# Kernel tuning notes

Measured on AMD Instinct MI355X. Metric: run time of the kernel, lower is better.

The kernel has to match this reference:

```python
import jax, jax.numpy as jnp
import numpy as np

EPS = 1e-5

def _conv1d(x, w, b):
    # x: [B, T, Cin]; w: [Cout, Cin, K] (torch layout); padding=1, stride=1
    y = jax.lax.conv_general_dilated(
        x, jnp.transpose(w, (2, 1, 0)), window_strides=(1,), padding=[(1, 1)],
        dimension_numbers=('NWC', 'WIO', 'NWC'))
    return y + b

def _layernorm(x, g, b):
    mu = jnp.mean(x, axis=-1, keepdims=True)
    var = jnp.mean(jnp.square(x - mu), axis=-1, keepdims=True)
    return (x - mu) * jax.lax.rsqrt(var + EPS) * g + b

def _predictor(x, conv1_w, conv1_b, ln1_g, ln1_b, conv2_w, conv2_b, ln2_g, ln2_b, lin_w, lin_b):
    h = _layernorm(jax.nn.relu(_conv1d(x, conv1_w, conv1_b)), ln1_g, ln1_b)
    h = _layernorm(jax.nn.relu(_conv1d(h, conv2_w, conv2_b)), ln2_g, ln2_b)
    # linear to 1 channel, relu, squeeze -> [B, T]
    return jax.nn.relu(jnp.einsum('btf,f->bt', h, lin_w[:, 0]) + lin_b[0])

def _length_regulate(x, durations, mel_max_length):
    # Equivalent to the one-hot alignment matmul: output frame p of batch b
    # copies token k where cumsum(dur)[k-1] <= p < cumsum(dur)[k]; zeros beyond total.
    B, T, D = x.shape
    cum = jnp.cumsum(durations, axis=-1)                       # [B, T]
    frames = jnp.arange(mel_max_length, dtype=cum.dtype)       # [M]
    idx = jax.vmap(lambda c: jnp.searchsorted(c, frames, side='right'))(cum)  # [B, M]
    idx = jnp.clip(idx, 0, T - 1)
    out = jnp.take_along_axis(x, idx[..., None], axis=1)       # [B, M, D]
    mask = (frames[None, :] < cum[:, -1:])                     # [B, M]
    return out * mask[..., None].astype(x.dtype)

def setup_inputs() -> dict:
    key = jax.random.key(0)
    ks = jax.random.split(key, 8)
    B, T, D, F = 32, 512, 256, 256
    M = 3584  # mel_max_length >= max possible sum of durations (7 * 512)
    x = jax.random.normal(ks[0], (B, T, D), dtype=jnp.float32)
    target = jax.random.randint(ks[1], (B, T), 0, 8, dtype=jnp.int32)
    s = 0.02
    return {
        'x': x,
        'conv1_w': jax.random.normal(ks[2], (F, D, 3), jnp.float32) * s,
        'conv1_b': jnp.zeros((F,), jnp.float32),
        'ln1_g': jnp.ones((F,), jnp.float32),
        'ln1_b': jnp.zeros((F,), jnp.float32),
        'conv2_w': jax.random.normal(ks[3], (F, F, 3), jnp.float32) * s,
        'conv2_b': jnp.zeros((F,), jnp.float32),
        'ln2_g': jnp.ones((F,), jnp.float32),
        'ln2_b': jnp.zeros((F,), jnp.float32),
        'lin_w': jax.random.normal(ks[4], (F, 1), jnp.float32) * s,
        'lin_b': jnp.zeros((1,), jnp.float32),
        'target': target,
        'mel_max_length': M,
    }

def reference(x, conv1_w, conv1_b, ln1_g, ln1_b, conv2_w, conv2_b, ln2_g, ln2_b, lin_w, lin_b, target, mel_max_length):
    dur_pred = _predictor(x, conv1_w, conv1_b, ln1_g, ln1_b, conv2_w, conv2_b, ln2_g, ln2_b, lin_w, lin_b)
    output = _length_regulate(x, target, mel_max_length)
    return output, dur_pred
```

## Files before the change

kernel.cpp:

```cpp
#include <hip/hip_runtime.h>
#include <hip/hip_bf16.h>

typedef float f32x4 __attribute__((ext_vector_type(4)));
typedef __bf16 bf16x8 __attribute__((ext_vector_type(8)));

static __device__ __forceinline__ unsigned short f2bf(float f) {
    unsigned int u = __float_as_uint(f);
    unsigned int r = (u + 0x7fffu + ((u >> 16) & 1u)) >> 16;
    return (unsigned short)r;
}

static __device__ __forceinline__ void gll16(const void* g, void* l) {
    __builtin_amdgcn_global_load_lds(
        (const __attribute__((address_space(1))) unsigned int*)g,
        (__attribute__((address_space(3))) unsigned int*)l, 16, 0, 0);
}

__global__ __launch_bounds__(512) void prep(
    const float* __restrict__ w1, const float* __restrict__ w2,
    unsigned short* __restrict__ w1p, unsigned short* __restrict__ w2p,
    const int* __restrict__ tgt, short* __restrict__ idxT, int M)
{
    int blk = blockIdx.x;
    if (blk < 256) {
        int gi = blk * 512 + threadIdx.x;
        const float* w = (gi < 65536) ? w1 : w2;
        unsigned short* wp = (gi < 65536) ? w1p : w2p;
        int p = gi & 65535;
        int n = p >> 8, cin = p & 255;
        const float* src = w + (size_t)p * 3;
        float a[3] = {src[0], src[1], src[2]};
        int nb = n >> 4, nl = n & 15;
        int e = cin & 7, lhi = (cin >> 3) & 3, chi = cin >> 5;
        int base = nb * 512 + (lhi * 16 + nl) * 8 + e;
        #pragma unroll
        for (int kk = 0; kk < 3; ++kk)
            wp[(kk * 8 + chi) * 8192 + base] = f2bf(a[kk]);
    } else {
        __shared__ int s[512];
        int b = blk - 256, tid = threadIdx.x;
        int d = tgt[b * 512 + tid];
        s[tid] = d;
        __syncthreads();
        for (int off = 1; off < 512; off <<= 1) {
            int v = (tid >= off) ? s[tid - off] : 0;
            __syncthreads();
            s[tid] += v;
            __syncthreads();
        }
        int myend = s[tid];
        int mystart = myend - d;
        short* row = idxT + (size_t)b * M;
        for (int p = mystart; p < myend; ++p) row[p] = (short)tid;
        __syncthreads();
        int total = s[511];
        for (int p = total + tid; p < M; p += 512) row[p] = (short)-1;
    }
}

static __device__ __forceinline__ void gather_part(
    int gblk, int jpb, int base, const float* __restrict__ x,
    const short* __restrict__ idxT, float* __restrict__ out, int M,
    int wv, int lane)
{
    int b = gblk / jpb;
    int r0 = (gblk - b * jpb) * 32 + base;
    const short* row = idxT + (size_t)b * M;
    int id[4];
    #pragma unroll
    for (int i = 0; i < 4; ++i) id[i] = row[r0 + i * 8 + wv];
    #pragma unroll
    for (int i = 0; i < 4; ++i) {
        int m = r0 + i * 8 + wv;
        float4 v = make_float4(0.f, 0.f, 0.f, 0.f);
        if (id[i] >= 0)
            v = *reinterpret_cast<const float4*>(x + ((size_t)(b * 512 + id[i])) * 256 + lane * 4);
        *reinterpret_cast<float4*>(out + ((size_t)b * M + m) * 256 + lane * 4) = v;
    }
}

__global__ __launch_bounds__(512, 4) void conv1_hetero(
    const float* __restrict__ x, const unsigned short* __restrict__ Wp,
    const float* __restrict__ bias, const float* __restrict__ g,
    const float* __restrict__ be, unsigned short* __restrict__ h1b,
    const short* __restrict__ idxT, float* __restrict__ out, int M)
{
    __shared__ __align__(16) unsigned short As[66 * 256];
    __shared__ __align__(16) unsigned short Bsm[2][8192];
    __shared__ float lnS[4][64], lnQ[4][64];

    const int tid = threadIdx.x;
    const int lane = tid & 63;
    const int wv = tid >> 6;

    if (blockIdx.x >= 256) {
        gather_part(blockIdx.x - 256, 68, 0, x, idxT, out, M, wv, lane);
        return;
    }

    const int wmi = wv >> 2, wni = wv & 3;
    const int grp = lane >> 4, lr = lane & 15;
    const int b = blockIdx.x >> 3;
    const int t_base = (blockIdx.x & 7) * 64;

    #pragma unroll
    for (int i = 0; i < 9; ++i) {
        int cc = i * 512 + tid;
        if (cc < 66 * 64) {
            int row = cc >> 6, q = cc & 63;
            int tt = t_base - 1 + row;
            ushort4 o = make_ushort4(0, 0, 0, 0);
            if ((unsigned)tt < 512u) {
                float4 v = *reinterpret_cast<const float4*>(x + ((size_t)(b * 512 + tt)) * 256 + q * 4);
                o.x = f2bf(v.x); o.y = f2bf(v.y); o.z = f2bf(v.z); o.w = f2bf(v.w);
            }
            *reinterpret_cast<ushort4*>(&As[row * 256 + ((q * 4) ^ ((row & 7) << 3))]) = o;
        }
    }

    const char* wpB = (const char*)Wp;
    char* bs0 = (char*)&Bsm[0][0];
    #define STAGE_B(kt, buf) do {                                              \
        const char* _s = wpB + (kt) * 16384 + wv * 2048 + lane * 16;           \
        char* _d = bs0 + (buf) * 16384 + wv * 2048;                            \
        gll16(_s, _d); gll16(_s + 1024, _d + 1024);                            \
    } while (0)

    STAGE_B(0, 0);
    __syncthreads();

    f32x4 acc[2][4] = {};
    int cur = 0;
    for (int kt = 0; kt < 24; ++kt) {
        if (kt < 23) STAGE_B(kt + 1, cur ^ 1);
        const int kk = kt >> 3, cin0 = (kt & 7) * 32;
        bf16x8 af[2], bfr[4];
        #pragma unroll
        for (int mi = 0; mi < 2; ++mi) {
            int tr = wmi * 32 + mi * 16 + lr + kk;
            af[mi] = *reinterpret_cast<const bf16x8*>(&As[tr * 256 + ((cin0 + grp * 8) ^ ((tr & 7) << 3))]);
        }
        #pragma unroll
        for (int ni = 0; ni < 4; ++ni)
            bfr[ni] = *reinterpret_cast<const bf16x8*>(&Bsm[cur][(wni * 4 + ni) * 512 + lane * 8]);
        __builtin_amdgcn_s_setprio(1);
        #pragma unroll
        for (int mi = 0; mi < 2; ++mi)
            #pragma unroll
            for (int ni = 0; ni < 4; ++ni)
                acc[mi][ni] = __builtin_amdgcn_mfma_f32_16x16x32_bf16(af[mi], bfr[ni], acc[mi][ni], 0, 0, 0);
        __builtin_amdgcn_s_setprio(0);
        __syncthreads();
        cur ^= 1;
    }

    float bcol[4], gcol[4], becol[4];
    #pragma unroll
    for (int ni = 0; ni < 4; ++ni) {
        int col = wni * 64 + ni * 16 + lr;
        bcol[ni] = bias[col]; gcol[ni] = g[col]; becol[ni] = be[col];
    }
    #pragma unroll
    for (int mi = 0; mi < 2; ++mi)
        #pragma unroll
        for (int ni = 0; ni < 4; ++ni)
            #pragma unroll
            for (int r = 0; r < 4; ++r)
                acc[mi][ni][r] = fmaxf(acc[mi][ni][r] + bcol[ni], 0.f);

    #pragma unroll
    for (int mi = 0; mi < 2; ++mi)
        #pragma unroll
        for (int r = 0; r < 4; ++r) {
            float s = acc[mi][0][r] + acc[mi][1][r] + acc[mi][2][r] + acc[mi][3][r];
            float q = acc[mi][0][r] * acc[mi][0][r] + acc[mi][1][r] * acc[mi][1][r]
                    + acc[mi][2][r] * acc[mi][2][r] + acc[mi][3][r] * acc[mi][3][r];
            #pragma unroll
            for (int off = 1; off < 16; off <<= 1) {
                s += __shfl_xor(s, off);
                q += __shfl_xor(q, off);
            }
            if (lr == 0) {
                int R = wmi * 32 + mi * 16 + grp * 4 + r;
                lnS[wni][R] = s; lnQ[wni][R] = q;
            }
        }
    __syncthreads();

    unsigned short* Hs = &Bsm[0][0];
    #pragma unroll
    for (int mi = 0; mi < 2; ++mi)
        #pragma unroll
        for (int r = 0; r < 4; ++r) {
            int R = wmi * 32 + mi * 16 + grp * 4 + r;
            float mu = (lnS[0][R] + lnS[1][R] + lnS[2][R] + lnS[3][R]) * (1.f / 256.f);
            float var = (lnQ[0][R] + lnQ[1][R] + lnQ[2][R] + lnQ[3][R]) * (1.f / 256.f) - mu * mu;
            float rs = rsqrtf(var + 1e-5f);
            #pragma unroll
            for (int ni = 0; ni < 4; ++ni) {
                int col = wni * 64 + ni * 16 + lr;
                float h = (acc[mi][ni][r] - mu) * rs * gcol[ni] + becol[ni];
                Hs[R * 256 + (col ^ ((R & 7) << 3))] = f2bf(h);
            }
        }
    __syncthreads();
    #pragma unroll
    for (int i = 0; i < 4; ++i) {
        int c = i * 512 + tid;
        int row = c >> 5, seg = c & 31;
        uint4 v = *reinterpret_cast<const uint4*>(&Hs[row * 256 + seg * 8]);
        *reinterpret_cast<uint4*>(h1b + ((size_t)(b * 512 + t_base + row)) * 256 + seg * 8) = v;
    }
    #undef STAGE_B
}

__global__ __launch_bounds__(512, 4) void conv2_hetero(
    const unsigned short* __restrict__ h1b, const unsigned short* __restrict__ Wp,
    const float* __restrict__ bias, const float* __restrict__ g,
    const float* __restrict__ be, const float* __restrict__ lw,
    const float* __restrict__ lb, float* __restrict__ dur,
    const short* __restrict__ idxT, const float* __restrict__ x,
    float* __restrict__ out, int M)
{
    __shared__ __align__(16) unsigned short As[66 * 256];
    __shared__ __align__(16) unsigned short Bsm[2][8192];
    __shared__ float lnS[4][64], lnQ[4][64], lnD[4][64];

    const int tid = threadIdx.x;
    const int lane = tid & 63;
    const int wv = tid >> 6;

    if (blockIdx.x >= 256) {
        gather_part(blockIdx.x - 256, 44, 2176, x, idxT, out, M, wv, lane);
        return;
    }

    const int wmi = wv >> 2, wni = wv & 3;
    const int grp = lane >> 4, lr = lane & 15;
    const int b = blockIdx.x >> 3;
    const int t_base = (blockIdx.x & 7) * 64;

    {
        const char* src = (const char*)h1b + ((size_t)(b * 512 + t_base)) * 512 + wv * 4096 + lane * 16;
        char* dst = (char*)&As[256] + wv * 4096;
        #pragma unroll
        for (int i = 0; i < 4; ++i) gll16(src + i * 1024, dst + i * 1024);
    }
    if (tid < 32) {
        int tt = t_base - 1;
        uint4 v = make_uint4(0u, 0u, 0u, 0u);
        if (tt >= 0)
            v = *reinterpret_cast<const uint4*>((const char*)h1b + ((size_t)(b * 512 + tt)) * 512 + tid * 16);
        *reinterpret_cast<uint4*>((char*)As + tid * 16) = v;
    } else if (tid < 64) {
        int t2 = tid - 32, tt = t_base + 64;
        uint4 v = make_uint4(0u, 0u, 0u, 0u);
        if (tt < 512)
            v = *reinterpret_cast<const uint4*>((const char*)h1b + ((size_t)(b * 512 + tt)) * 512 + t2 * 16);
        *reinterpret_cast<uint4*>((char*)&As[65 * 256] + t2 * 16) = v;
    }

    const char* wpB = (const char*)Wp;
    char* bs0 = (char*)&Bsm[0][0];
    #define STAGE_B(kt, buf) do {                                              \
        const char* _s = wpB + (kt) * 16384 + wv * 2048 + lane * 16;           \
        char* _d = bs0 + (buf) * 16384 + wv * 2048;                            \
        gll16(_s, _d); gll16(_s + 1024, _d + 1024);                            \
    } while (0)

    STAGE_B(0, 0);
    __syncthreads();

    f32x4 acc[2][4] = {};
    int cur = 0;
    for (int kt = 0; kt < 24; ++kt) {
        if (kt < 23) STAGE_B(kt + 1, cur ^ 1);
        const int kk = kt >> 3, cin0 = (kt & 7) * 32;
        bf16x8 af[2], bfr[4];
        #pragma unroll
        for (int mi = 0; mi < 2; ++mi) {
            int tr = wmi * 32 + mi * 16 + lr + kk;
            af[mi] = *reinterpret_cast<const bf16x8*>(&As[tr * 256 + ((cin0 + grp * 8) ^ (((tr + 7) & 7) << 3))]);
        }
        #pragma unroll
        for (int ni = 0; ni < 4; ++ni)
            bfr[ni] = *reinterpret_cast<const bf16x8*>(&Bsm[cur][(wni * 4 + ni) * 512 + lane * 8]);
        __builtin_amdgcn_s_setprio(1);
        #pragma unroll
        for (int mi = 0; mi < 2; ++mi)
            #pragma unroll
            for (int ni = 0; ni < 4; ++ni)
                acc[mi][ni] = __builtin_amdgcn_mfma_f32_16x16x32_bf16(af[mi], bfr[ni], acc[mi][ni], 0, 0, 0);
        __builtin_amdgcn_s_setprio(0);
        __syncthreads();
        cur ^= 1;
    }

    float bcol[4], gcol[4], becol[4], wcol[4];
    #pragma unroll
    for (int ni = 0; ni < 4; ++ni) {
        int col = wni * 64 + ni * 16 + lr;
        bcol[ni] = bias[col]; gcol[ni] = g[col]; becol[ni] = be[col]; wcol[ni] = lw[col];
    }
    #pragma unroll
    for (int mi = 0; mi < 2; ++mi)
        #pragma unroll
        for (int ni = 0; ni < 4; ++ni)
            #pragma unroll
            for (int r = 0; r < 4; ++r)
                acc[mi][ni][r] = fmaxf(acc[mi][ni][r] + bcol[ni], 0.f);

    #pragma unroll
    for (int mi = 0; mi < 2; ++mi)
        #pragma unroll
        for (int r = 0; r < 4; ++r) {
            float s = acc[mi][0][r] + acc[mi][1][r] + acc[mi][2][r] + acc[mi][3][r];
            float q = acc[mi][0][r] * acc[mi][0][r] + acc[mi][1][r] * acc[mi][1][r]
                    + acc[mi][2][r] * acc[mi][2][r] + acc[mi][3][r] * acc[mi][3][r];
            #pragma unroll
            for (int off = 1; off < 16; off <<= 1) {
                s += __shfl_xor(s, off);
                q += __shfl_xor(q, off);
            }
            if (lr == 0) {
                int R = wmi * 32 + mi * 16 + grp * 4 + r;
                lnS[wni][R] = s; lnQ[wni][R] = q;
            }
        }
    __syncthreads();
    #pragma unroll
    for (int mi = 0; mi < 2; ++mi)
        #pragma unroll
        for (int r = 0; r < 4; ++r) {
            int R = wmi * 32 + mi * 16 + grp * 4 + r;
            float mu = (lnS[0][R] + lnS[1][R] + lnS[2][R] + lnS[3][R]) * (1.f / 256.f);
            float var = (lnQ[0][R] + lnQ[1][R] + lnQ[2][R] + lnQ[3][R]) * (1.f / 256.f) - mu * mu;
            float rs = rsqrtf(var + 1e-5f);
            float d = ((acc[mi][0][r] - mu) * rs * gcol[0] + becol[0]) * wcol[0]
                    + ((acc[mi][1][r] - mu) * rs * gcol[1] + becol[1]) * wcol[1]
                    + ((acc[mi][2][r] - mu) * rs * gcol[2] + becol[2]) * wcol[2]
                    + ((acc[mi][3][r] - mu) * rs * gcol[3] + becol[3]) * wcol[3];
            #pragma unroll
            for (int off = 1; off < 16; off <<= 1) d += __shfl_xor(d, off);
            if (lr == 0) lnD[wni][R] = d;
        }
    __syncthreads();
    if (tid < 64) {
        float dd = lnD[0][tid] + lnD[1][tid] + lnD[2][tid] + lnD[3][tid] + lb[0];
        dur[(size_t)b * 512 + t_base + tid] = fmaxf(dd, 0.f);
    }
    #undef STAGE_B
}

extern "C" void kernel_launch(void* const* d_in, const int* in_sizes, int n_in,
                              void* d_out, int out_size, void* d_ws, size_t ws_size,
                              hipStream_t stream) {
    const float* x   = (const float*)d_in[0];
    const float* w1  = (const float*)d_in[1];
    const float* b1  = (const float*)d_in[2];
    const float* g1  = (const float*)d_in[3];
    const float* be1 = (const float*)d_in[4];
    const float* w2  = (const float*)d_in[5];
    const float* b2  = (const float*)d_in[6];
    const float* g2  = (const float*)d_in[7];
    const float* be2 = (const float*)d_in[8];
    const float* lw  = (const float*)d_in[9];
    const float* lb  = (const float*)d_in[10];
    const int* tgt   = (const int*)d_in[11];
    float* out = (float*)d_out;

    const int B = 32, T = 512, C = 256;
    const int rows = B * T;
    const int M = (out_size - rows) / (B * C);

    char* ws = (char*)d_ws;
    unsigned short* w1p = (unsigned short*)(ws);
    unsigned short* w2p = (unsigned short*)(ws + 393216);
    unsigned short* h1b = (unsigned short*)(ws + 786432);
    short* idxT         = (short*)(ws + 9175040);

    prep<<<288, 512, 0, stream>>>(w1, w2, w1p, w2p, tgt, idxT, M);
    conv1_hetero<<<2432, 512, 0, stream>>>(x, w1p, b1, g1, be1, h1b, idxT, out, M);
    conv2_hetero<<<1664, 512, 0, stream>>>(h1b, w2p, b2, g2, be2, lw, lb,
                                           out + (size_t)B * M * C, idxT, x, out, M);
}
```

Measured before the change: 57.97 us.

## Split conv A-tile staging into two channel halves to halve LDS footprint

Both conv kernels now stage the activation tile in two 128-channel halves instead of loading all 256 channels at once. This halves the As shared buffer so LDS use per block drops, which may let more blocks or gather work fit per CU. The K loop is reordered so each half runs 12 steps over the matching weight tiles. The cost is an extra tile reload, an extra barrier, and a pipeline restart between halves.

```diff
diff --git a/kernel.cpp b/kernel.cpp
--- a/kernel.cpp
+++ b/kernel.cpp
@@ -85,7 +85,7 @@
     const float* __restrict__ be, unsigned short* __restrict__ h1b,
     const short* __restrict__ idxT, float* __restrict__ out, int M)
 {
-    __shared__ __align__(16) unsigned short As[66 * 256];
+    __shared__ __align__(16) unsigned short As[66 * 128];
     __shared__ __align__(16) unsigned short Bsm[2][8192];
     __shared__ float lnS[4][64], lnQ[4][64];
 
@@ -103,55 +103,62 @@
     const int b = blockIdx.x >> 3;
     const int t_base = (blockIdx.x & 7) * 64;
 
-    #pragma unroll
-    for (int i = 0; i < 9; ++i) {
-        int cc = i * 512 + tid;
-        if (cc < 66 * 64) {
-            int row = cc >> 6, q = cc & 63;
-            int tt = t_base - 1 + row;
-            ushort4 o = make_ushort4(0, 0, 0, 0);
-            if ((unsigned)tt < 512u) {
-                float4 v = *reinterpret_cast<const float4*>(x + ((size_t)(b * 512 + tt)) * 256 + q * 4);
-                o.x = f2bf(v.x); o.y = f2bf(v.y); o.z = f2bf(v.z); o.w = f2bf(v.w);
-            }
-            *reinterpret_cast<ushort4*>(&As[row * 256 + ((q * 4) ^ ((row & 7) << 3))]) = o;
-        }
-    }
-
     const char* wpB = (const char*)Wp;
     char* bs0 = (char*)&Bsm[0][0];
-    #define STAGE_B(kt, buf) do {                                              \
-        const char* _s = wpB + (kt) * 16384 + wv * 2048 + lane * 16;           \
+    #define STAGE_B(ktg, buf) do {                                             \
+        const char* _s = wpB + (ktg) * 16384 + wv * 2048 + lane * 16;          \
         char* _d = bs0 + (buf) * 16384 + wv * 2048;                            \
         gll16(_s, _d); gll16(_s + 1024, _d + 1024);                            \
     } while (0)
 
-    STAGE_B(0, 0);
-    __syncthreads();
-
     f32x4 acc[2][4] = {};
     int cur = 0;
-    for (int kt = 0; kt < 24; ++kt) {
-        if (kt < 23) STAGE_B(kt + 1, cur ^ 1);
-        const int kk = kt >> 3, cin0 = (kt & 7) * 32;
-        bf16x8 af[2], bfr[4];
-        #pragma unroll
-        for (int mi = 0; mi < 2; ++mi) {
-            int tr = wmi * 32 + mi * 16 + lr + kk;
-            af[mi] = *reinterpret_cast<const bf16x8*>(&As[tr * 256 + ((cin0 + grp * 8) ^ ((tr & 7) << 3))]);
-        }
-        #pragma unroll
-        for (int ni = 0; ni < 4; ++ni)
-            bfr[ni] = *reinterpret_cast<const bf16x8*>(&Bsm[cur][(wni * 4 + ni) * 512 + lane * 8]);
-        __builtin_amdgcn_s_setprio(1);
-        #pragma unroll
-        for (int mi = 0; mi < 2; ++mi)
+
+    for (int h = 0; h < 2; ++h) {
+        #pragma unroll
+        for (int i = 0; i < 5; ++i) {
+            int cc = i * 512 + tid;
+            if (cc < 66 * 32) {
+                int row = cc >> 5, ql = cc & 31;
+                int tt = t_base - 1 + row;
+                ushort4 o = make_ushort4(0, 0, 0, 0);
+                if ((unsigned)tt < 512u) {
+                    float4 v = *reinterpret_cast<const float4*>(
+                        x + ((size_t)(b * 512 + tt)) * 256 + h * 128 + ql * 4);
+                    o.x = f2bf(v.x); o.y = f2bf(v.y); o.z = f2bf(v.z); o.w = f2bf(v.w);
+                }
+                *reinterpret_cast<ushort4*>(&As[row * 128 + ((ql * 4) ^ ((row & 7) << 3))]) = o;
+            }
+        }
+        STAGE_B(h * 4, cur);
+        __syncthreads();
+
+        for (int j = 0; j < 12; ++j) {
+            if (j < 11) {
+                int jn = j + 1;
+                STAGE_B((jn >> 2) * 8 + h * 4 + (jn & 3), cur ^ 1);
+            }
+            const int cbl = j & 3, kk = j >> 2;
+            bf16x8 af[2], bfr[4];
+            #pragma unroll
+            for (int mi = 0; mi < 2; ++mi) {
+                int tr = wmi * 32 + mi * 16 + lr + kk;
+                af[mi] = *reinterpret_cast<const bf16x8*>(
+                    &As[tr * 128 + ((cbl * 32 + grp * 8) ^ ((tr & 7) << 3))]);
+            }
             #pragma unroll
             for (int ni = 0; ni < 4; ++ni)
-                acc[mi][ni] = __builtin_amdgcn_mfma_f32_16x16x32_bf16(af[mi], bfr[ni], acc[mi][ni], 0, 0, 0);
-        __builtin_amdgcn_s_setprio(0);
-        __syncthreads();
-        cur ^= 1;
+                bfr[ni] = *reinterpret_cast<const bf16x8*>(&Bsm[cur][(wni * 4 + ni) * 512 + lane * 8]);
+            __builtin_amdgcn_s_setprio(1);
+            #pragma unroll
+            for (int mi = 0; mi < 2; ++mi)
+                #pragma unroll
+                for (int ni = 0; ni < 4; ++ni)
+                    acc[mi][ni] = __builtin_amdgcn_mfma_f32_16x16x32_bf16(af[mi], bfr[ni], acc[mi][ni], 0, 0, 0);
+            __builtin_amdgcn_s_setprio(0);
+            __syncthreads();
+            cur ^= 1;
+        }
     }
 
     float bcol[4], gcol[4], becol[4];
@@ -199,8 +206,8 @@
             #pragma unroll
             for (int ni = 0; ni < 4; ++ni) {
                 int col = wni * 64 + ni * 16 + lr;
-                float h = (acc[mi][ni][r] - mu) * rs * gcol[ni] + becol[ni];
-                Hs[R * 256 + (col ^ ((R & 7) << 3))] = f2bf(h);
+                float hv = (acc[mi][ni][r] - mu) * rs * gcol[ni] + becol[ni];
+                Hs[R * 256 + (col ^ ((R & 7) << 3))] = f2bf(hv);
             }
         }
     __syncthreads();
@@ -222,7 +229,7 @@
     const short* __restrict__ idxT, const float* __restrict__ x,
     float* __restrict__ out, int M)
 {
-    __shared__ __align__(16) unsigned short As[66 * 256];
+    __shared__ __align__(16) unsigned short As[66 * 128];
     __shared__ __align__(16) unsigned short Bsm[2][8192];
     __shared__ float lnS[4][64], lnQ[4][64], lnD[4][64];
 
@@ -240,60 +247,69 @@
     const int b = blockIdx.x >> 3;
     const int t_base = (blockIdx.x & 7) * 64;
 
-    {
-        const char* src = (const char*)h1b + ((size_t)(b * 512 + t_base)) * 512 + wv * 4096 + lane * 16;
-        char* dst = (char*)&As[256] + wv * 4096;
-        #pragma unroll
-        for (int i = 0; i < 4; ++i) gll16(src + i * 1024, dst + i * 1024);
-    }
-    if (tid < 32) {
-        int tt = t_base - 1;
-        uint4 v = make_uint4(0u, 0u, 0u, 0u);
-        if (tt >= 0)
-            v = *reinterpret_cast<const uint4*>((const char*)h1b + ((size_t)(b * 512 + tt)) * 512 + tid * 16);
-        *reinterpret_cast<uint4*>((char*)As + tid * 16) = v;
-    } else if (tid < 64) {
-        int t2 = tid - 32, tt = t_base + 64;
-        uint4 v = make_uint4(0u, 0u, 0u, 0u);
-        if (tt < 512)
-            v = *reinterpret_cast<const uint4*>((const char*)h1b + ((size_t)(b * 512 + tt)) * 512 + t2 * 16);
-        *reinterpret_cast<uint4*>((char*)&As[65 * 256] + t2 * 16) = v;
-    }
-
     const char* wpB = (const char*)Wp;
+    const char* h1B = (const char*)h1b;
     char* bs0 = (char*)&Bsm[0][0];
-    #define STAGE_B(kt, buf) do {                                              \
-        const char* _s = wpB + (kt) * 16384 + wv * 2048 + lane * 16;           \
+    #define STAGE_B(ktg, buf) do {                                             \
+        const char* _s = wpB + (ktg) * 16384 + wv * 2048 + lane * 16;          \
         char* _d = bs0 + (buf) * 16384 + wv * 2048;                            \
         gll16(_s, _d); gll16(_s + 1024, _d + 1024);                            \
     } while (0)
 
-    STAGE_B(0, 0);
-    __syncthreads();
-
     f32x4 acc[2][4] = {};
     int cur = 0;
-    for (int kt = 0; kt < 24; ++kt) {
-        if (kt < 23) STAGE_B(kt + 1, cur ^ 1);
-        const int kk = kt >> 3, cin0 = (kt & 7) * 32;
-        bf16x8 af[2], bfr[4];
-        #pragma unroll
-        for (int mi = 0; mi < 2; ++mi) {
-            int tr = wmi * 32 + mi * 16 + lr + kk;
-            af[mi] = *reinterpret_cast<const bf16x8*>(&As[tr * 256 + ((cin0 + grp * 8) ^ (((tr + 7) & 7) << 3))]);
-        }
-        #pragma unroll
-        for (int ni = 0; ni < 4; ++ni)
-            bfr[ni] = *reinterpret_cast<const bf16x8*>(&Bsm[cur][(wni * 4 + ni) * 512 + lane * 8]);
-        __builtin_amdgcn_s_setprio(1);
-        #pragma unroll
-        for (int mi = 0; mi < 2; ++mi)
+
+    for (int h = 0; h < 2; ++h) {
+        #pragma unroll
+        for (int j2 = 0; j2 < 2; ++j2) {
+            int row0 = 1 + wv * 8 + j2 * 4;
+            const char* src = h1B
+                + ((size_t)(b * 512 + t_base + wv * 8 + j2 * 4 + (lane >> 4))) * 512
+                + h * 256 + (lane & 15) * 16;
+            gll16(src, (char*)As + row0 * 256);
+        }
+        if (tid < 16) {
+            int tt = t_base - 1;
+            uint4 v = make_uint4(0u, 0u, 0u, 0u);
+            if (tt >= 0)
+                v = *reinterpret_cast<const uint4*>(h1B + ((size_t)(b * 512 + tt)) * 512 + h * 256 + tid * 16);
+            *reinterpret_cast<uint4*>((char*)As + tid * 16) = v;
+        } else if (tid < 32) {
+            int t2 = tid - 16, tt = t_base + 64;
+            uint4 v = make_uint4(0u, 0u, 0u, 0u);
+            if (tt < 512)
+                v = *reinterpret_cast<const uint4*>(h1B + ((size_t)(b * 512 + tt)) * 512 + h * 256 + t2 * 16);
+            *reinterpret_cast<uint4*>((char*)As + 65 * 256 + t2 * 16) = v;
+        }
+        STAGE_B(h * 4, cur);
+        __syncthreads();
+
+        for (int j = 0; j < 12; ++j) {
+            if (j < 11) {
+                int jn = j + 1;
+                STAGE_B((jn >> 2) * 8 + h * 4 + (jn & 3), cur ^ 1);
+            }
+            const int cbl = j & 3, kk = j >> 2;
+            bf16x8 af[2], bfr[4];
+            #pragma unroll
+            for (int mi = 0; mi < 2; ++mi) {
+                int tr = wmi * 32 + mi * 16 + lr + kk;
+                af[mi] = *reinterpret_cast<const bf16x8*>(
+                    &As[tr * 128 + ((cbl * 32 + grp * 8) ^ (((tr + 7) & 7) << 3))]);
+            }
             #pragma unroll
             for (int ni = 0; ni < 4; ++ni)
-                acc[mi][ni] = __builtin_amdgcn_mfma_f32_16x16x32_bf16(af[mi], bfr[ni], acc[mi][ni], 0, 0, 0);
-        __builtin_amdgcn_s_setprio(0);
-        __syncthreads();
-        cur ^= 1;
+                bfr[ni] = *reinterpret_cast<const bf16x8*>(&Bsm[cur][(wni * 4 + ni) * 512 + lane * 8]);
+            __builtin_amdgcn_s_setprio(1);
+            #pragma unroll
+            for (int mi = 0; mi < 2; ++mi)
+                #pragma unroll
+                for (int ni = 0; ni < 4; ++ni)
+                    acc[mi][ni] = __builtin_amdgcn_mfma_f32_16x16x32_bf16(af[mi], bfr[ni], acc[mi][ni], 0, 0, 0);
+            __builtin_amdgcn_s_setprio(0);
+            __syncthreads();
+            cur ^= 1;
+        }
     }
 
     float bcol[4], gcol[4], becol[4], wcol[4];
```

Measured after the change: 57.87 us. Within noise of the previous version (-0.2%).

## Fuse both conv+layernorm stages into one kernel with halo recompute

Applied to the files above, without the earlier changes.

Merges the conv1 and conv2 kernels into a single kernel. Each block computes conv1 over 64 rows (62 outputs plus a halo on each side) and keeps the normalized intermediate in shared memory, so the bf16 h1 round-trip through global memory and one kernel launch go away. The conv1 input is staged in four 64-channel chunks to fit LDS, and the gather work is rebalanced into 64-row chunks appended after 288 compute blocks. The cost is about 3% extra conv1 compute for the halo rows and higher LDS use per block, which may reduce occupancy.

```diff
diff --git a/kernel.cpp b/kernel.cpp
--- a/kernel.cpp
+++ b/kernel.cpp
@@ -58,296 +58,253 @@
     }
 }
 
-static __device__ __forceinline__ void gather_part(
-    int gblk, int jpb, int base, const float* __restrict__ x,
-    const short* __restrict__ idxT, float* __restrict__ out, int M,
-    int wv, int lane)
+__global__ __launch_bounds__(512, 4) void fused(
+    const float* __restrict__ x,
+    const unsigned short* __restrict__ w1p, const float* __restrict__ b1,
+    const float* __restrict__ g1, const float* __restrict__ be1,
+    const unsigned short* __restrict__ w2p, const float* __restrict__ b2,
+    const float* __restrict__ g2, const float* __restrict__ be2,
+    const float* __restrict__ lw, const float* __restrict__ lb,
+    float* __restrict__ dur, const short* __restrict__ idxT,
+    float* __restrict__ out, int M)
 {
-    int b = gblk / jpb;
-    int r0 = (gblk - b * jpb) * 32 + base;
-    const short* row = idxT + (size_t)b * M;
-    int id[4];
-    #pragma unroll
-    for (int i = 0; i < 4; ++i) id[i] = row[r0 + i * 8 + wv];
-    #pragma unroll
-    for (int i = 0; i < 4; ++i) {
-        int m = r0 + i * 8 + wv;
-        float4 v = make_float4(0.f, 0.f, 0.f, 0.f);
-        if (id[i] >= 0)
-            v = *reinterpret_cast<const float4*>(x + ((size_t)(b * 512 + id[i])) * 256 + lane * 4);
-        *reinterpret_cast<float4*>(out + ((size_t)b * M + m) * 256 + lane * 4) = v;
-    }
-}
-
-__global__ __launch_bounds__(512, 4) void conv1_hetero(
-    const float* __restrict__ x, const unsigned short* __restrict__ Wp,
-    const float* __restrict__ bias, const float* __restrict__ g,
-    const float* __restrict__ be, unsigned short* __restrict__ h1b,
-    const short* __restrict__ idxT, float* __restrict__ out, int M)
-{
-    __shared__ __align__(16) unsigned short As[66 * 256];
+    __shared__ __align__(16) unsigned short H[64 * 256];
+    __shared__ __align__(16) unsigned short As[66 * 64];
     __shared__ __align__(16) unsigned short Bsm[2][8192];
-    __shared__ float lnS[4][64], lnQ[4][64];
+    __shared__ float lnS[4][64], lnQ[4][64], lnD[4][64];
 
     const int tid = threadIdx.x;
     const int lane = tid & 63;
     const int wv = tid >> 6;
 
-    if (blockIdx.x >= 256) {
-        gather_part(blockIdx.x - 256, 68, 0, x, idxT, out, M, wv, lane);
+    if (blockIdx.x >= 288) {
+        int gid = blockIdx.x - 288;
+        int b = gid / 56;
+        int r0 = (gid - b * 56) * 64;
+        const short* row = idxT + (size_t)b * M;
+        int id[8];
+        #pragma unroll
+        for (int i = 0; i < 8; ++i) id[i] = row[r0 + i * 8 + wv];
+        #pragma unroll
+        for (int i = 0; i < 8; ++i) {
+            int m = r0 + i * 8 + wv;
+            float4 v = make_float4(0.f, 0.f, 0.f, 0.f);
+            if (id[i] >= 0)
+                v = *reinterpret_cast<const float4*>(x + ((size_t)(b * 512 + id[i])) * 256 + lane * 4);
+            *reinterpret_cast<float4*>(out + ((size_t)b * M + m) * 256 + lane * 4) = v;
+        }
         return;
     }
 
     const int wmi = wv >> 2, wni = wv & 3;
     const int grp = lane >> 4, lr = lane & 15;
-    const int b = blockIdx.x >> 3;
-    const int t_base = (blockIdx.x & 7) * 64;
-
-    #pragma unroll
-    for (int i = 0; i < 9; ++i) {
-        int cc = i * 512 + tid;
-        if (cc < 66 * 64) {
-            int row = cc >> 6, q = cc & 63;
-            int tt = t_base - 1 + row;
-            ushort4 o = make_ushort4(0, 0, 0, 0);
-            if ((unsigned)tt < 512u) {
-                float4 v = *reinterpret_cast<const float4*>(x + ((size_t)(b * 512 + tt)) * 256 + q * 4);
-                o.x = f2bf(v.x); o.y = f2bf(v.y); o.z = f2bf(v.z); o.w = f2bf(v.w);
-            }
-            *reinterpret_cast<ushort4*>(&As[row * 256 + ((q * 4) ^ ((row & 7) << 3))]) = o;
-        }
-    }
-
-    const char* wpB = (const char*)Wp;
+    const int b = blockIdx.x / 9;
+    const int t0 = (blockIdx.x - b * 9) * 62;
+
     char* bs0 = (char*)&Bsm[0][0];
-    #define STAGE_B(kt, buf) do {                                              \
-        const char* _s = wpB + (kt) * 16384 + wv * 2048 + lane * 16;           \
+    #define STAGE_B(basep, ktg, buf) do {                                      \
+        const char* _s = (const char*)(basep) + (ktg) * 16384 + wv * 2048 + lane * 16; \
         char* _d = bs0 + (buf) * 16384 + wv * 2048;                            \
         gll16(_s, _d); gll16(_s + 1024, _d + 1024);                            \
     } while (0)
 
-    STAGE_B(0, 0);
-    __syncthreads();
-
     f32x4 acc[2][4] = {};
     int cur = 0;
-    for (int kt = 0; kt < 24; ++kt) {
-        if (kt < 23) STAGE_B(kt + 1, cur ^ 1);
-        const int kk = kt >> 3, cin0 = (kt & 7) * 32;
-        bf16x8 af[2], bfr[4];
-        #pragma unroll
-        for (int mi = 0; mi < 2; ++mi) {
-            int tr = wmi * 32 + mi * 16 + lr + kk;
-            af[mi] = *reinterpret_cast<const bf16x8*>(&As[tr * 256 + ((cin0 + grp * 8) ^ ((tr & 7) << 3))]);
-        }
-        #pragma unroll
-        for (int ni = 0; ni < 4; ++ni)
-            bfr[ni] = *reinterpret_cast<const bf16x8*>(&Bsm[cur][(wni * 4 + ni) * 512 + lane * 8]);
-        __builtin_amdgcn_s_setprio(1);
-        #pragma unroll
-        for (int mi = 0; mi < 2; ++mi)
+    for (int h = 0; h < 4; ++h) {
+        #pragma unroll
+        for (int i = 0; i < 3; ++i) {
+            int cc = i * 512 + tid;
+            if (cc < 66 * 16) {
+                int row = cc >> 4, ql = cc & 15;
+                int tt = t0 - 2 + row;
+                ushort4 o = make_ushort4(0, 0, 0, 0);
+                if ((unsigned)tt < 512u) {
+                    float4 v = *reinterpret_cast<const float4*>(
+                        x + ((size_t)(b * 512 + tt)) * 256 + h * 64 + ql * 4);
+                    o.x = f2bf(v.x); o.y = f2bf(v.y); o.z = f2bf(v.z); o.w = f2bf(v.w);
+                }
+                *reinterpret_cast<ushort4*>(&As[row * 64 + ((ql * 4) ^ ((row & 7) << 3))]) = o;
+            }
+        }
+        if (h == 0) STAGE_B(w1p, 0, cur);
+        __syncthreads();
+
+        for (int j = 0; j < 6; ++j) {
+            if (j < 5) {
+                int jn = j + 1;
+                STAGE_B(w1p, (jn >> 1) * 8 + h * 2 + (jn & 1), cur ^ 1);
+            } else if (h < 3) {
+                STAGE_B(w1p, (h + 1) * 2, cur ^ 1);
+            } else {
+                STAGE_B(w2p, 0, cur ^ 1);
+            }
+            const int kk = j >> 1, cbl = j & 1;
+            bf16x8 af[2], bfr[4];
+            #pragma unroll
+            for (int mi = 0; mi < 2; ++mi) {
+                int tr = wmi * 32 + mi * 16 + lr + kk;
+                af[mi] = *reinterpret_cast<const bf16x8*>(
+                    &As[tr * 64 + ((cbl * 32 + grp * 8) ^ ((tr & 7) << 3))]);
+            }
             #pragma unroll
             for (int ni = 0; ni < 4; ++ni)
-                acc[mi][ni] = __builtin_amdgcn_mfma_f32_16x16x32_bf16(af[mi], bfr[ni], acc[mi][ni], 0, 0, 0);
-        __builtin_amdgcn_s_setprio(0);
-        __syncthreads();
-        cur ^= 1;
-    }
-
-    float bcol[4], gcol[4], becol[4];
-    #pragma unroll
-    for (int ni = 0; ni < 4; ++ni) {
-        int col = wni * 64 + ni * 16 + lr;
-        bcol[ni] = bias[col]; gcol[ni] = g[col]; becol[ni] = be[col];
-    }
-    #pragma unroll
-    for (int mi = 0; mi < 2; ++mi)
-        #pragma unroll
-        for (int ni = 0; ni < 4; ++ni)
-            #pragma unroll
-            for (int r = 0; r < 4; ++r)
-                acc[mi][ni][r] = fmaxf(acc[mi][ni][r] + bcol[ni], 0.f);
-
-    #pragma unroll
-    for (int mi = 0; mi < 2; ++mi)
-        #pragma unroll
-        for (int r = 0; r < 4; ++r) {
-            float s = acc[mi][0][r] + acc[mi][1][r] + acc[mi][2][r] + acc[mi][3][r];
-            float q = acc[mi][0][r] * acc[mi][0][r] + acc[mi][1][r] * acc[mi][1][r]
-                    + acc[mi][2][r] * acc[mi][2][r] + acc[mi][3][r] * acc[mi][3][r];
-            #pragma unroll
-            for (int off = 1; off < 16; off <<= 1) {
-                s += __shfl_xor(s, off);
-                q += __shfl_xor(q, off);
-            }
-            if (lr == 0) {
+                bfr[ni] = *reinterpret_cast<const bf16x8*>(&Bsm[cur][(wni * 4 + ni) * 512 + lane * 8]);
+            __builtin_amdgcn_s_setprio(1);
+            #pragma unroll
+            for (int mi = 0; mi < 2; ++mi)
+                #pragma unroll
+                for (int ni = 0; ni < 4; ++ni)
+                    acc[mi][ni] = __builtin_amdgcn_mfma_f32_16x16x32_bf16(af[mi], bfr[ni], acc[mi][ni], 0, 0, 0);
+            __builtin_amdgcn_s_setprio(0);
+            __syncthreads();
+            cur ^= 1;
+        }
+    }
+
+    {
+        float bcol[4], gcol[4], becol[4];
+        #pragma unroll
+        for (int ni = 0; ni < 4; ++ni) {
+            int col = wni * 64 + ni * 16 + lr;
+            bcol[ni] = b1[col]; gcol[ni] = g1[col]; becol[ni] = be1[col];
+        }
+        #pragma unroll
+        for (int mi = 0; mi < 2; ++mi)
+            #pragma unroll
+            for (int ni = 0; ni < 4; ++ni)
+                #pragma unroll
+                for (int r = 0; r < 4; ++r)
+                    acc[mi][ni][r] = fmaxf(acc[mi][ni][r] + bcol[ni], 0.f);
+
+        #pragma unroll
+        for (int mi = 0; mi < 2; ++mi)
+            #pragma unroll
+            for (int r = 0; r < 4; ++r) {
+                float s = acc[mi][0][r] + acc[mi][1][r] + acc[mi][2][r] + acc[mi][3][r];
+                float q = acc[mi][0][r] * acc[mi][0][r] + acc[mi][1][r] * acc[mi][1][r]
+                        + acc[mi][2][r] * acc[mi][2][r] + acc[mi][3][r] * acc[mi][3][r];
+                #pragma unroll
+                for (int off = 1; off < 16; off <<= 1) {
+                    s += __shfl_xor(s, off);
+                    q += __shfl_xor(q, off);
+                }
+                if (lr == 0) {
+                    int R = wmi * 32 + mi * 16 + grp * 4 + r;
+                    lnS[wni][R] = s; lnQ[wni][R] = q;
+                }
+            }
+        __syncthreads();
+        #pragma unroll
+        for (int mi = 0; mi < 2; ++mi)
+            #pragma unroll
+            for (int r = 0; r < 4; ++r) {
                 int R = wmi * 32 + mi * 16 + grp * 4 + r;
-                lnS[wni][R] = s; lnQ[wni][R] = q;
-            }
-        }
-    __syncthreads();
-
-    unsigned short* Hs = &Bsm[0][0];
-    #pragma unroll
-    for (int mi = 0; mi < 2; ++mi)
-        #pragma unroll
-        for (int r = 0; r < 4; ++r) {
-            int R = wmi * 32 + mi * 16 + grp * 4 + r;
-            float mu = (lnS[0][R] + lnS[1][R] + lnS[2][R] + lnS[3][R]) * (1.f / 256.f);
-            float var = (lnQ[0][R] + lnQ[1][R] + lnQ[2][R] + lnQ[3][R]) * (1.f / 256.f) - mu * mu;
-            float rs = rsqrtf(var + 1e-5f);
-            #pragma unroll
-            for (int ni = 0; ni < 4; ++ni) {
-                int col = wni * 64 + ni * 16 + lr;
-                float h = (acc[mi][ni][r] - mu) * rs * gcol[ni] + becol[ni];
-                Hs[R * 256 + (col ^ ((R & 7) << 3))] = f2bf(h);
-            }
-        }
-    __syncthreads();
-    #pragma unroll
-    for (int i = 0; i < 4; ++i) {
-        int c = i * 512 + tid;
-        int row = c >> 5, seg = c & 31;
-        uint4 v = *reinterpret_cast<const uint4*>(&Hs[row * 256 + seg * 8]);
-        *reinterpret_cast<uint4*>(h1b + ((size_t)(b * 512 + t_base + row)) * 256 + seg * 8) = v;
-    }
-    #undef STAGE_B
-}
-
-__global__ __launch_bounds__(512, 4) void conv2_hetero(
-    const unsigned short* __restrict__ h1b, const unsigned short* __restrict__ Wp,
-    const float* __restrict__ bias, const float* __restrict__ g,
-    const float* __restrict__ be, const float* __restrict__ lw,
-    const float* __restrict__ lb, float* __restrict__ dur,
-    const short* __restrict__ idxT, const float* __restrict__ x,
-    float* __restrict__ out, int M)
-{
-    __shared__ __align__(16) unsigned short As[66 * 256];
-    __shared__ __align__(16) unsigned short Bsm[2][8192];
-    __shared__ float lnS[4][64], lnQ[4][64], lnD[4][64];
-
-    const int tid = threadIdx.x;
-    const int lane = tid & 63;
-    const int wv = tid >> 6;
-
-    if (blockIdx.x >= 256) {
-        gather_part(blockIdx.x - 256, 44, 2176, x, idxT, out, M, wv, lane);
-        return;
-    }
-
-    const int wmi = wv >> 2, wni = wv & 3;
-    const int grp = lane >> 4, lr = lane & 15;
-    const int b = blockIdx.x >> 3;
-    const int t_base = (blockIdx.x & 7) * 64;
+                int t = t0 - 1 + R;
+                float valid = ((unsigned)t < 512u) ? 1.f : 0.f;
+                float mu = (lnS[0][R] + lnS[1][R] + lnS[2][R] + lnS[3][R]) * (1.f / 256.f);
+                float var = (lnQ[0][R] + lnQ[1][R] + lnQ[2][R] + lnQ[3][R]) * (1.f / 256.f) - mu * mu;
+                float rs = rsqrtf(var + 1e-5f);
+                #pragma unroll
+                for (int ni = 0; ni < 4; ++ni) {
+                    int col = wni * 64 + ni * 16 + lr;
+                    float hv = ((acc[mi][ni][r] - mu) * rs * gcol[ni] + becol[ni]) * valid;
+                    H[R * 256 + (col ^ ((R & 7) << 3))] = f2bf(hv);
+                }
+            }
+        __syncthreads();
+    }
+
+    f32x4 acc2[2][4] = {};
+    for (int h = 0; h < 4; ++h) {
+        for (int j = 0; j < 6; ++j) {
+            if (j < 5) {
+                int jn = j + 1;
+                STAGE_B(w2p, (jn >> 1) * 8 + h * 2 + (jn & 1), cur ^ 1);
+            } else if (h < 3) {
+                STAGE_B(w2p, (h + 1) * 2, cur ^ 1);
+            }
+            const int kk = j >> 1, cbl = j & 1;
+            bf16x8 af[2], bfr[4];
+            #pragma unroll
+            for (int mi = 0; mi < 2; ++mi) {
+                int tr = wmi * 32 + mi * 16 + lr + kk - 1;
+                int trc = tr < 0 ? 0 : (tr > 63 ? 63 : tr);
+                af[mi] = *reinterpret_cast<const bf16x8*>(
+                    &H[trc * 256 + ((h * 64 + cbl * 32 + grp * 8) ^ ((trc & 7) << 3))]);
+            }
+            #pragma unroll
+            for (int ni = 0; ni < 4; ++ni)
+                bfr[ni] = *reinterpret_cast<const bf16x8*>(&Bsm[cur][(wni * 4 + ni) * 512 + lane * 8]);
+            __builtin_amdgcn_s_setprio(1);
+            #pragma unroll
+            for (int mi = 0; mi < 2; ++mi)
+                #pragma unroll
+                for (int ni = 0; ni < 4; ++ni)
+                    acc2[mi][ni] = __builtin_amdgcn_mfma_f32_16x16x32_bf16(af[mi], bfr[ni], acc2[mi][ni], 0, 0, 0);
+            __builtin_amdgcn_s_setprio(0);
+            __syncthreads();
+            cur ^= 1;
+        }
+    }
 
     {
-        const char* src = (const char*)h1b + ((size_t)(b * 512 + t_base)) * 512 + wv * 4096 + lane * 16;
-        char* dst = (char*)&As[256] + wv * 4096;
-        #pragma unroll
-        for (int i = 0; i < 4; ++i) gll16(src + i * 1024, dst + i * 1024);
-    }
-    if (tid < 32) {
-        int tt = t_base - 1;
-        uint4 v = make_uint4(0u, 0u, 0u, 0u);
-        if (tt >= 0)
-            v = *reinterpret_cast<const uint4*>((const char*)h1b + ((size_t)(b * 512 + tt)) * 512 + tid * 16);
-        *reinterpret_cast<uint4*>((char*)As + tid * 16) = v;
-    } else if (tid < 64) {
-        int t2 = tid - 32, tt = t_base + 64;
-        uint4 v = make_uint4(0u, 0u, 0u, 0u);
-        if (tt < 512)
-            v = *reinterpret_cast<const uint4*>((const char*)h1b + ((size_t)(b * 512 + tt)) * 512 + t2 * 16);
-        *reinterpret_cast<uint4*>((char*)&As[65 * 256] + t2 * 16) = v;
-    }
-
-    const char* wpB = (const char*)Wp;
-    char* bs0 = (char*)&Bsm[0][0];
-    #define STAGE_B(kt, buf) do {                                              \
-        const char* _s = wpB + (kt) * 16384 + wv * 2048 + lane * 16;           \
-        char* _d = bs0 + (buf) * 16384 + wv * 2048;                            \
-        gll16(_s, _d); gll16(_s + 1024, _d + 1024);                            \
-    } while (0)
-
-    STAGE_B(0, 0);
-    __syncthreads();
-
-    f32x4 acc[2][4] = {};
-    int cur = 0;
-    for (int kt = 0; kt < 24; ++kt) {
-        if (kt < 23) STAGE_B(kt + 1, cur ^ 1);
-        const int kk = kt >> 3, cin0 = (kt & 7) * 32;
-        bf16x8 af[2], bfr[4];
-        #pragma unroll
-        for (int mi = 0; mi < 2; ++mi) {
-            int tr = wmi * 32 + mi * 16 + lr + kk;
-            af[mi] = *reinterpret_cast<const bf16x8*>(&As[tr * 256 + ((cin0 + grp * 8) ^ (((tr + 7) & 7) << 3))]);
-        }
-        #pragma unroll
-        for (int ni = 0; ni < 4; ++ni)
-            bfr[ni] = *reinterpret_cast<const bf16x8*>(&Bsm[cur][(wni * 4 + ni) * 512 + lane * 8]);
-        __builtin_amdgcn_s_setprio(1);
+        float bcol[4], gcol[4], becol[4], wcol[4];
+        #pragma unroll
+        for (int ni = 0; ni < 4; ++ni) {
+            int col = wni * 64 + ni * 16 + lr;
+            bcol[ni] = b2[col]; gcol[ni] = g2[col]; becol[ni] = be2[col]; wcol[ni] = lw[col];
+        }
         #pragma unroll
         for (int mi = 0; mi < 2; ++mi)
             #pragma unroll
             for (int ni = 0; ni < 4; ++ni)
-                acc[mi][ni] = __builtin_amdgcn_mfma_f32_16x16x32_bf16(af[mi], bfr[ni], acc[mi][ni], 0, 0, 0);
-        __builtin_amdgcn_s_setprio(0);
-        __syncthreads();
-        cur ^= 1;
-    }
-
-    float bcol[4], gcol[4], becol[4], wcol[4];
-    #pragma unroll
-    for (int ni = 0; ni < 4; ++ni) {
-        int col = wni * 64 + ni * 16 + lr;
-        bcol[ni] = bias[col]; gcol[ni] = g[col]; becol[ni] = be[col]; wcol[ni] = lw[col];
-    }
-    #pragma unroll
-    for (int mi = 0; mi < 2; ++mi)
-        #pragma unroll
-        for (int ni = 0; ni < 4; ++ni)
-            #pragma unroll
-            for (int r = 0; r < 4; ++r)
-                acc[mi][ni][r] = fmaxf(acc[mi][ni][r] + bcol[ni], 0.f);
-
-    #pragma unroll
-    for (int mi = 0; mi < 2; ++mi)
-        #pragma unroll
-        for (int r = 0; r < 4; ++r) {
-            float s = acc[mi][0][r] + acc[mi][1][r] + acc[mi][2][r] + acc[mi][3][r];
-            float q = acc[mi][0][r] * acc[mi][0][r] + acc[mi][1][r] * acc[mi][1][r]
-                    + acc[mi][2][r] * acc[mi][2][r] + acc[mi][3][r] * acc[mi][3][r];
-            #pragma unroll
-            for (int off = 1; off < 16; off <<= 1) {
-                s += __shfl_xor(s, off);
-                q += __shfl_xor(q, off);
-            }
-            if (lr == 0) {
+                #pragma unroll
+                for (int r = 0; r < 4; ++r)
+                    acc2[mi][ni][r] = fmaxf(acc2[mi][ni][r] + bcol[ni], 0.f);
+
+        #pragma unroll
+        for (int mi = 0; mi < 2; ++mi)
+            #pragma unroll
+            for (int r = 0; r < 4; ++r) {
+                float s = acc2[mi][0][r] + acc2[mi][1][r] + acc2[mi][2][r] + acc2[mi][3][r];
+                float q = acc2[mi][0][r] * acc2[mi][0][r] + acc2[mi][1][r] * acc2[mi][1][r]
+                        + acc2[mi][2][r] * acc2[mi][2][r] + acc2[mi][3][r] * acc2[mi][3][r];
+                #pragma unroll
+                for (int off = 1; off < 16; off <<= 1) {
+                    s += __shfl_xor(s, off);
+                    q += __shfl_xor(q, off);
+                }
+                if (lr == 0) {
+                    int R = wmi * 32 + mi * 16 + grp * 4 + r;
+                    lnS[wni][R] = s; lnQ[wni][R] = q;
+                }
+            }
+        __syncthreads();
+        #pragma unroll
+        for (int mi = 0; mi < 2; ++mi)
+            #pragma unroll
+            for (int r = 0; r < 4; ++r) {
                 int R = wmi * 32 + mi * 16 + grp * 4 + r;
-                lnS[wni][R] = s; lnQ[wni][R] = q;
-            }
-        }
-    __syncthreads();
-    #pragma unroll
-    for (int mi = 0; mi < 2; ++mi)
-        #pragma unroll
-        for (int r = 0; r < 4; ++r) {
-            int R = wmi * 32 + mi * 16 + grp * 4 + r;
-            float mu = (lnS[0][R] + lnS[1][R] + lnS[2][R] + lnS[3][R]) * (1.f / 256.f);
-            float var = (lnQ[0][R] + lnQ[1][R] + lnQ[2][R] + lnQ[3][R]) * (1.f / 256.f) - mu * mu;
-            float rs = rsqrtf(var + 1e-5f);
-            float d = ((acc[mi][0][r] - mu) * rs * gcol[0] + becol[0]) * wcol[0]
-                    + ((acc[mi][1][r] - mu) * rs * gcol[1] + becol[1]) * wcol[1]
-                    + ((acc[mi][2][r] - mu) * rs * gcol[2] + becol[2]) * wcol[2]
-                    + ((acc[mi][3][r] - mu) * rs * gcol[3] + becol[3]) * wcol[3];
-            #pragma unroll
-            for (int off = 1; off < 16; off <<= 1) d += __shfl_xor(d, off);
-            if (lr == 0) lnD[wni][R] = d;
-        }
-    __syncthreads();
-    if (tid < 64) {
-        float dd = lnD[0][tid] + lnD[1][tid] + lnD[2][tid] + lnD[3][tid] + lb[0];
-        dur[(size_t)b * 512 + t_base + tid] = fmaxf(dd, 0.f);
+                float mu = (lnS[0][R] + lnS[1][R] + lnS[2][R] + lnS[3][R]) * (1.f / 256.f);
+                float var = (lnQ[0][R] + lnQ[1][R] + lnQ[2][R] + lnQ[3][R]) * (1.f / 256.f) - mu * mu;
+                float rs = rsqrtf(var + 1e-5f);
+                float d = ((acc2[mi][0][r] - mu) * rs * gcol[0] + becol[0]) * wcol[0]
+                        + ((acc2[mi][1][r] - mu) * rs * gcol[1] + becol[1]) * wcol[1]
+                        + ((acc2[mi][2][r] - mu) * rs * gcol[2] + becol[2]) * wcol[2]
+                        + ((acc2[mi][3][r] - mu) * rs * gcol[3] + becol[3]) * wcol[3];
+                #pragma unroll
+                for (int off = 1; off < 16; off <<= 1) d += __shfl_xor(d, off);
+                if (lr == 0) lnD[wni][R] = d;
+            }
+        __syncthreads();
+        if (tid < 64) {
+            int R = tid;
+            int t = t0 - 1 + R;
+            if (R >= 1 && R <= 62 && t < 512) {
+                float dd = lnD[0][R] + lnD[1][R] + lnD[2][R] + lnD[3][R] + lb[0];
+                dur[(size_t)b * 512 + t] = fmaxf(dd, 0.f);
+            }
+        }
     }
     #undef STAGE_B
 }
@@ -376,11 +333,9 @@
     char* ws = (char*)d_ws;
     unsigned short* w1p = (unsigned short*)(ws);
     unsigned short* w2p = (unsigned short*)(ws + 393216);
-    unsigned short* h1b = (unsigned short*)(ws + 786432);
-    short* idxT         = (short*)(ws + 9175040);
+    short* idxT         = (short*)(ws + 786432);
 
     prep<<<288, 512, 0, stream>>>(w1, w2, w1p, w2p, tgt, idxT, M);
-    conv1_hetero<<<2432, 512, 0, stream>>>(x, w1p, b1, g1, be1, h1b, idxT, out, M);
-    conv2_hetero<<<1664, 512, 0, stream>>>(h1b, w2p, b2, g2, be2, lw, lb,
-                                           out + (size_t)B * M * C, idxT, x, out, M);
-}
+    fused<<<2080, 512, 0, stream>>>(x, w1p, b1, g1, be1, w2p, b2, g2, be2,
+                                    lw, lb, out + (size_t)B * M * C, idxT, out, M);
+}
```

New measurement: 53.55 us. 1.08x faster.
